# Optimization experiments

Measured on AMD Instinct MI355X. Metric: run time of the kernel, lower is better.

Reference implementation:

```python
import jax, jax.numpy as jnp
import numpy as np

N_EMB, D_LAT, D_HID, D_MID, D_IN = 1024, 64, 256, 128, 9
BETA = 0.25  # commitment_cost
N = 262144


def _kaiming(k, shape):
    # kaiming_normal_ with nonlinearity='relu': std = sqrt(2 / fan_in)
    fan_in = shape[1]
    return jax.random.normal(k, shape, jnp.float32) * jnp.sqrt(jnp.float32(2.0 / fan_in))


def setup_inputs() -> dict:
    key = jax.random.key(0)
    ks = jax.random.split(key, 8)
    return {
        "x": jax.random.normal(ks[0], (N, D_IN), jnp.float32),
        # Encoder: Linear(9->256) ReLU Linear(256->128) ReLU Linear(128->64)
        "enc_w1": _kaiming(ks[1], (D_HID, D_IN)),  "enc_b1": jnp.zeros((D_HID,), jnp.float32),
        "enc_w2": _kaiming(ks[2], (D_MID, D_HID)), "enc_b2": jnp.zeros((D_MID,), jnp.float32),
        "enc_w3": _kaiming(ks[3], (D_LAT, D_MID)), "enc_b3": jnp.zeros((D_LAT,), jnp.float32),
        # Decoder: Linear(64->128) ReLU Linear(128->256) ReLU Linear(256->9)
        "dec_w1": _kaiming(ks[4], (D_MID, D_LAT)), "dec_b1": jnp.zeros((D_MID,), jnp.float32),
        "dec_w2": _kaiming(ks[5], (D_HID, D_MID)), "dec_b2": jnp.zeros((D_HID,), jnp.float32),
        "dec_w3": _kaiming(ks[6], (D_IN, D_HID)),  "dec_b3": jnp.zeros((D_IN,), jnp.float32),
        # Codebook: Embedding(1024, 64), uniform(-1, 1)
        "codebook": jax.random.uniform(ks[7], (N_EMB, D_LAT), jnp.float32, -1.0, 1.0),
    }


def _mlp3(h, w1, b1, w2, b2, w3, b3):
    h = jax.nn.relu(h @ w1.T + b1)
    h = jax.nn.relu(h @ w2.T + b2)
    return h @ w3.T + b3


def reference(x, enc_w1, enc_b1, enc_w2, enc_b2, enc_w3, enc_b3,
              dec_w1, dec_b1, dec_w2, dec_b2, dec_w3, dec_b3, codebook):
    z_e = _mlp3(x, enc_w1, enc_b1, enc_w2, enc_b2, enc_w3, enc_b3)  # [N, 64]
    # squared euclidean distances to codebook: [N, N_EMB]
    d = (jnp.sum(z_e * z_e, axis=1, keepdims=True)
         - 2.0 * (z_e @ codebook.T)
         + jnp.sum(codebook * codebook, axis=1))
    idx = jnp.argmin(d, axis=1)                 # [N] int
    quantized = codebook[idx]                   # gather == onehot @ codebook
    e_latent = jnp.mean((jax.lax.stop_gradient(quantized) - z_e) ** 2)
    q_latent = jnp.mean((quantized - jax.lax.stop_gradient(z_e)) ** 2)
    vq_loss = q_latent + BETA * e_latent
    # straight-through estimator
    z_q = z_e + jax.lax.stop_gradient(quantized - z_e)
    # perplexity from codebook usage histogram (== mean of one-hot encodings)
    counts = jnp.zeros((N_EMB,), jnp.float32).at[idx].add(1.0)
    avg_probs = counts / jnp.float32(z_e.shape[0])
    perplexity = jnp.exp(-jnp.sum(avg_probs * jnp.log(avg_probs + 1e-10)))
    x_recon = _mlp3(z_q, dec_w1, dec_b1, dec_w2, dec_b2, dec_w3, dec_b3)
    return (x_recon, vq_loss, perplexity)
```

## Files before the change

kernel.cpp:

```cpp
#include <hip/hip_runtime.h>
#include <math.h>


namespace {

constexpr int kN = 262144;

typedef _Float16 half8 __attribute__((ext_vector_type(8)));
typedef float floatx4 __attribute__((ext_vector_type(4)));

#define MFMA16(a, b, c) __builtin_amdgcn_mfma_f32_16x16x32_f16((a), (b), (c), 0, 0, 0)
#define LDS_FENCE() asm volatile("s_waitcnt lgkmcnt(0)" ::: "memory")
#define VMCNT0() asm volatile("s_waitcnt vmcnt(0)" ::: "memory")
#define BARRIER()                                  \
  do {                                             \
    asm volatile("" ::: "memory");                 \
    __builtin_amdgcn_s_barrier();                  \
    asm volatile("" ::: "memory");                 \
  } while (0)

constexpr size_t W1M_O = 0;
constexpr size_t W1R_O = 16384;
constexpr size_t E2M_O = 32768;
constexpr size_t E2R_O = 98304;
constexpr size_t E3M_O = 163840;
constexpr size_t E3R_O = 180224;
constexpr size_t CBM_O = 196608;
constexpr size_t CBR_O = 327680;
constexpr size_t D1P_O = 458752;
constexpr size_t D2P_O = 475136;
constexpr size_t D3P_O = 540672;
constexpr size_t CN_O  = 548864;
constexpr size_t IDX_O = 589824;
constexpr size_t ESP_O = IDX_O + 1048576;
constexpr size_t HP_O  = ESP_O + 32768;

__device__ __forceinline__ void split2(float v, _Float16& hi, _Float16& lo) {
  hi = (_Float16)v;
  lo = (_Float16)(v - (float)hi);
}

__global__ void prep_kernel(
    const float* __restrict__ ew1, const float* __restrict__ ew2,
    const float* __restrict__ ew3, const float* __restrict__ cb,
    const float* __restrict__ dw1, const float* __restrict__ dw2,
    const float* __restrict__ dw3, char* __restrict__ wsb) {
  _Float16* w1m = (_Float16*)(wsb + W1M_O);
  _Float16* w1r = (_Float16*)(wsb + W1R_O);
  _Float16* e2m = (_Float16*)(wsb + E2M_O);
  _Float16* e2r = (_Float16*)(wsb + E2R_O);
  _Float16* e3m = (_Float16*)(wsb + E3M_O);
  _Float16* e3r = (_Float16*)(wsb + E3R_O);
  _Float16* cbm = (_Float16*)(wsb + CBM_O);
  _Float16* cbr = (_Float16*)(wsb + CBR_O);
  _Float16* d1p = (_Float16*)(wsb + D1P_O);
  _Float16* d2p = (_Float16*)(wsb + D2P_O);
  _Float16* d3p = (_Float16*)(wsb + D3P_O);
  float* cn = (float*)(wsb + CN_O);

  const int gid = blockIdx.x * 256 + threadIdx.x;
  const int stride = gridDim.x * 256;
  for (int e = gid; e < 256 * 32; e += stride) {
    int n = e >> 5, k = e & 31;
    float v = (k < 9) ? ew1[n * 9 + k] : 0.f;
    split2(v, w1m[e], w1r[e]);
  }
  for (int e = gid; e < 128 * 256; e += stride) split2(ew2[e], e2m[e], e2r[e]);
  for (int e = gid; e < 64 * 128; e += stride) split2(ew3[e], e3m[e], e3r[e]);
  for (int e = gid; e < 1024 * 64; e += stride) split2(cb[e], cbm[e], cbr[e]);
  for (int e = gid; e < 128 * 64; e += stride) d1p[e] = (_Float16)dw1[e];
  for (int e = gid; e < 256 * 128; e += stride) d2p[e] = (_Float16)dw2[e];
  for (int e = gid; e < 16 * 256; e += stride) {
    int n = e >> 8, k = e & 255;
    d3p[e] = (n < 9) ? (_Float16)dw3[n * 256 + k] : (_Float16)0.f;
  }
  for (int i = gid; i < 1024; i += stride) {
    float s = 0.f;
    const float* c = cb + (size_t)i * 64;
#pragma unroll 8
    for (int k = 0; k < 64; ++k) s = fmaf(c[k], c[k], s);
    cn[i] = s;
  }
}

__global__ __launch_bounds__(256, 3) void vqvae_mega(
    const float* __restrict__ x,
    const float* __restrict__ eb1, const float* __restrict__ eb2,
    const float* __restrict__ eb3, const float* __restrict__ db1,
    const float* __restrict__ db2, const float* __restrict__ db3,
    const float* __restrict__ cb, const char* __restrict__ wsb,
    float* __restrict__ out, int* __restrict__ idx_g, float* __restrict__ esp_g) {
  __shared__ _Float16 LP[20480];

  const int t = threadIdx.x;
  const int lane = t & 63;
  const int w = t >> 6;
  const int m = lane & 15;
  const int q = lane >> 4;
  const int R0 = blockIdx.x * 128;
  const int wr0 = 32 * w;
  _Float16* WPS = LP + 10240 + w * 2560;
  const float* cn_g = (const float*)(wsb + CN_O);

  half8 axm[2] = {{}, {}}, axr[2] = {{}, {}};
#pragma unroll
  for (int rt = 0; rt < 2; ++rt) {
    const int grow = R0 + wr0 + 16 * rt + m;
    if (q == 0) {
#pragma unroll
      for (int j = 0; j < 8; ++j) {
        const float v = x[(size_t)grow * 9 + j];
        const _Float16 hi = (_Float16)v;
        axm[rt][j] = hi;
        axr[rt][j] = (_Float16)(v - (float)hi);
      }
    } else if (q == 1) {
      const float v = x[(size_t)grow * 9 + 8];
      const _Float16 hi = (_Float16)v;
      axm[rt][0] = hi;
      axr[rt][0] = (_Float16)(v - (float)hi);
    }
  }

  floatx4 acc2[8][2];
#pragma unroll
  for (int nt = 0; nt < 8; ++nt)
#pragma unroll
    for (int rt = 0; rt < 2; ++rt) acc2[nt][rt] = (floatx4){0.f, 0.f, 0.f, 0.f};

  {
    const int pA = t >> 7, nA = t & 127;
    const char* srcA = wsb + (pA ? E2R_O : E2M_O) + (size_t)nA * 512;
    _Float16* dstA = LP + (pA ? 5120 : 0) + nA * 40;
    half8 stg[4];
#pragma unroll
    for (int j = 0; j < 4; ++j) stg[j] = *(const half8*)(srcA + j * 16);

    for (int kc = 0; kc < 8; ++kc) {
      VMCNT0();
#pragma unroll
      for (int j = 0; j < 4; ++j) *(half8*)(dstA + j * 8) = stg[j];
      LDS_FENCE();
      if (kc < 7) {
#pragma unroll
        for (int j = 0; j < 4; ++j)
          stg[j] = *(const half8*)(srcA + (size_t)(kc + 1) * 64 + j * 16);
      }
      BARRIER();

#pragma unroll
      for (int ntl = 0; ntl < 2; ++ntl) {
        const int f = kc * 32 + ntl * 16 + m;
        const half8 bm = *(const half8*)(wsb + W1M_O + (size_t)f * 64 + q * 16);
        const half8 br = *(const half8*)(wsb + W1R_O + (size_t)f * 64 + q * 16);
        const float bias = eb1[f];
#pragma unroll
        for (int rt = 0; rt < 2; ++rt) {
          floatx4 a = (floatx4){0.f, 0.f, 0.f, 0.f};
          a = MFMA16(axr[rt], bm, a);
          a = MFMA16(axm[rt], br, a);
          a = MFMA16(axm[rt], bm, a);
#pragma unroll
          for (int reg = 0; reg < 4; ++reg) {
            const float v = fmaxf(a[reg] + bias, 0.f);
            const int row = 16 * rt + 4 * q + reg;
            const _Float16 hi = (_Float16)v;
            WPS[row * 40 + ntl * 16 + m] = hi;
            WPS[1280 + row * 40 + ntl * 16 + m] = (_Float16)(v - (float)hi);
          }
        }
      }
      LDS_FENCE();
      half8 am[2], ar[2];
#pragma unroll
      for (int rt = 0; rt < 2; ++rt) {
        am[rt] = *(const half8*)(WPS + (16 * rt + m) * 40 + q * 8);
        ar[rt] = *(const half8*)(WPS + 1280 + (16 * rt + m) * 40 + q * 8);
      }
#pragma unroll
      for (int nt = 0; nt < 8; ++nt) {
        const half8 bm = *(const half8*)(LP + (nt * 16 + m) * 40 + q * 8);
        const half8 br = *(const half8*)(LP + 5120 + (nt * 16 + m) * 40 + q * 8);
#pragma unroll
        for (int rt = 0; rt < 2; ++rt) {
          acc2[nt][rt] = MFMA16(ar[rt], bm, acc2[nt][rt]);
          acc2[nt][rt] = MFMA16(am[rt], br, acc2[nt][rt]);
          acc2[nt][rt] = MFMA16(am[rt], bm, acc2[nt][rt]);
        }
      }
      BARRIER();
    }
  }

  floatx4 acc3[4][2];
#pragma unroll
  for (int nt = 0; nt < 4; ++nt)
#pragma unroll
    for (int rt = 0; rt < 2; ++rt) acc3[nt][rt] = (floatx4){0.f, 0.f, 0.f, 0.f};

  for (int ks = 0; ks < 4; ++ks) {
#pragma unroll
    for (int h = 0; h < 2; ++h) {
      const int nt = 2 * ks + h;
      const float bias = eb2[nt * 16 + m];
#pragma unroll
      for (int rt = 0; rt < 2; ++rt) {
#pragma unroll
        for (int reg = 0; reg < 4; ++reg) {
          const float v = fmaxf(acc2[nt][rt][reg] + bias, 0.f);
          const int row = 16 * rt + 4 * q + reg;
          const _Float16 hi = (_Float16)v;
          WPS[row * 40 + h * 16 + m] = hi;
          WPS[1280 + row * 40 + h * 16 + m] = (_Float16)(v - (float)hi);
        }
      }
    }
    LDS_FENCE();
    half8 am[2], ar[2];
#pragma unroll
    for (int rt = 0; rt < 2; ++rt) {
      am[rt] = *(const half8*)(WPS + (16 * rt + m) * 40 + q * 8);
      ar[rt] = *(const half8*)(WPS + 1280 + (16 * rt + m) * 40 + q * 8);
    }
#pragma unroll
    for (int nt = 0; nt < 4; ++nt) {
      const half8 bm = *(const half8*)(wsb + E3M_O + (size_t)(nt * 16 + m) * 256 + ks * 64 + q * 16);
      const half8 br = *(const half8*)(wsb + E3R_O + (size_t)(nt * 16 + m) * 256 + ks * 64 + q * 16);
#pragma unroll
      for (int rt = 0; rt < 2; ++rt) {
        acc3[nt][rt] = MFMA16(ar[rt], bm, acc3[nt][rt]);
        acc3[nt][rt] = MFMA16(am[rt], br, acc3[nt][rt]);
        acc3[nt][rt] = MFMA16(am[rt], bm, acc3[nt][rt]);
      }
    }
  }

  const int pC = t >> 7, eC = t & 127;
  const int nC = eC >> 1, hC = eC & 1;
  const char* srcC = wsb + (pC ? CBR_O : CBM_O) + (size_t)nC * 128 + hC * 64;
  _Float16* dstC = LP + (pC ? 4608 : 0) + nC * 72 + hC * 32;
  half8 stgC[4];
#pragma unroll
  for (int j = 0; j < 4; ++j) stgC[j] = *(const half8*)(srcC + j * 16);

  half8 zfm[2][2], zfr[2][2];
#pragma unroll
  for (int rt = 0; rt < 2; ++rt) {
#pragma unroll
    for (int nt = 0; nt < 4; ++nt) {
      const float bias = eb3[nt * 16 + m];
#pragma unroll
      for (int reg = 0; reg < 4; ++reg) {
        const float v = acc3[nt][rt][reg] + bias;
        const int row = 4 * q + reg;
        const _Float16 hi = (_Float16)v;
        WPS[row * 72 + nt * 16 + m] = hi;
        WPS[1152 + row * 72 + nt * 16 + m] = (_Float16)(v - (float)hi);
      }
    }
    LDS_FENCE();
#pragma unroll
    for (int ks2 = 0; ks2 < 2; ++ks2) {
      zfm[rt][ks2] = *(const half8*)(WPS + m * 72 + ks2 * 32 + q * 8);
      zfr[rt][ks2] = *(const half8*)(WPS + 1152 + m * 72 + ks2 * 32 + q * 8);
    }
  }

  float bestd[2][4];
  int besti[2][4];
#pragma unroll
  for (int rt = 0; rt < 2; ++rt)
#pragma unroll
    for (int reg = 0; reg < 4; ++reg) { bestd[rt][reg] = 3.4e38f; besti[rt][reg] = 0; }

  for (int cc = 0; cc < 16; ++cc) {
    VMCNT0();
#pragma unroll
    for (int j = 0; j < 4; ++j) *(half8*)(dstC + j * 8) = stgC[j];
    LDS_FENCE();
    if (cc < 15) {
#pragma unroll
      for (int j = 0; j < 4; ++j)
        stgC[j] = *(const half8*)(srcC + (size_t)(cc + 1) * 8192 + j * 16);
    }
    BARRIER();

    floatx4 accd[4][2];
#pragma unroll
    for (int nt = 0; nt < 4; ++nt)
#pragma unroll
      for (int rt = 0; rt < 2; ++rt) accd[nt][rt] = (floatx4){0.f, 0.f, 0.f, 0.f};
#pragma unroll
    for (int nt = 0; nt < 4; ++nt) {
#pragma unroll
      for (int ks2 = 0; ks2 < 2; ++ks2) {
        const half8 bm = *(const half8*)(LP + (nt * 16 + m) * 72 + ks2 * 32 + q * 8);
        const half8 br = *(const half8*)(LP + 4608 + (nt * 16 + m) * 72 + ks2 * 32 + q * 8);
#pragma unroll
        for (int rt = 0; rt < 2; ++rt) {
          accd[nt][rt] = MFMA16(zfr[rt][ks2], bm, accd[nt][rt]);
          accd[nt][rt] = MFMA16(zfm[rt][ks2], br, accd[nt][rt]);
          accd[nt][rt] = MFMA16(zfm[rt][ks2], bm, accd[nt][rt]);
        }
      }
    }
#pragma unroll
    for (int nt = 0; nt < 4; ++nt) {
      const int code = cc * 64 + nt * 16 + m;
      const float cnv = cn_g[code];
#pragma unroll
      for (int rt = 0; rt < 2; ++rt) {
#pragma unroll
        for (int reg = 0; reg < 4; ++reg) {
          const float d = cnv - 2.f * accd[nt][rt][reg];
          if (d < bestd[rt][reg]) { bestd[rt][reg] = d; besti[rt][reg] = code; }
        }
      }
    }
    BARRIER();
  }
#pragma unroll
  for (int rt = 0; rt < 2; ++rt) {
#pragma unroll
    for (int reg = 0; reg < 4; ++reg) {
#pragma unroll
      for (int off = 1; off < 16; off <<= 1) {
        const float od = __shfl_xor(bestd[rt][reg], off, 16);
        const int oi = __shfl_xor(besti[rt][reg], off, 16);
        if (od < bestd[rt][reg] || (od == bestd[rt][reg] && oi < besti[rt][reg])) {
          bestd[rt][reg] = od; besti[rt][reg] = oi;
        }
      }
    }
  }
  if (m == 0) {
#pragma unroll
    for (int rt = 0; rt < 2; ++rt)
#pragma unroll
      for (int reg = 0; reg < 4; ++reg) {
        const int row = wr0 + 16 * rt + 4 * q + reg;
        idx_g[R0 + row] = besti[rt][reg];
      }
  }

  const int sl = ((m >> 2) << 4) | m;
  half8 zq[2][2];
  float es = 0.f;
#pragma unroll
  for (int rt = 0; rt < 2; ++rt) {
    const int b0 = __shfl(besti[rt][0], sl);
    const int b1 = __shfl(besti[rt][1], sl);
    const int b2 = __shfl(besti[rt][2], sl);
    const int b3 = __shfl(besti[rt][3], sl);
    const int r2 = m & 3;
    const int bi = (r2 == 0) ? b0 : (r2 == 1) ? b1 : (r2 == 2) ? b2 : b3;
#pragma unroll
    for (int ks2 = 0; ks2 < 2; ++ks2) {
      const float* cp = cb + (size_t)bi * 64 + ks2 * 32 + q * 8;
      const float4 c0 = *(const float4*)cp;
      const float4 c1 = *(const float4*)(cp + 4);
      float cv[8] = {c0.x, c0.y, c0.z, c0.w, c1.x, c1.y, c1.z, c1.w};
#pragma unroll
      for (int j = 0; j < 8; ++j) {
        const float z = (float)zfm[rt][ks2][j] + (float)zfr[rt][ks2][j];
        const float d = cv[j] - z;
        es = fmaf(d, d, es);
        zq[rt][ks2][j] = (_Float16)(z + d);
      }
    }
  }
#pragma unroll
  for (int off = 1; off < 64; off <<= 1) es += __shfl_xor(es, off, 64);
  if (lane == 0) esp_g[blockIdx.x * 4 + w] = es;

  const int nE = t >> 2, jE = t & 3;
  const char* srcE = wsb + D2P_O + (size_t)nE * 256 + jE * 64;
  _Float16* dstE = LP + nE * 136 + jE * 32;
  half8 stgE[4];
#pragma unroll
  for (int j = 0; j < 4; ++j) stgE[j] = *(const half8*)(srcE + j * 16);

  floatx4 accH[8][2];
#pragma unroll
  for (int nt = 0; nt < 8; ++nt)
#pragma unroll
    for (int rt = 0; rt < 2; ++rt) accH[nt][rt] = (floatx4){0.f, 0.f, 0.f, 0.f};
#pragma unroll
  for (int nt = 0; nt < 8; ++nt) {
#pragma unroll
    for (int ks2 = 0; ks2 < 2; ++ks2) {
      const half8 b = *(const half8*)(wsb + D1P_O + (size_t)(nt * 16 + m) * 128 + ks2 * 64 + q * 16);
#pragma unroll
      for (int rt = 0; rt < 2; ++rt) accH[nt][rt] = MFMA16(zq[rt][ks2], b, accH[nt][rt]);
    }
  }
  half8 h3f[2][4];
  for (int ks = 0; ks < 4; ++ks) {
#pragma unroll
    for (int h = 0; h < 2; ++h) {
      const int nt = 2 * ks + h;
      const float bias = db1[nt * 16 + m];
#pragma unroll
      for (int rt = 0; rt < 2; ++rt)
#pragma unroll
        for (int reg = 0; reg < 4; ++reg) {
          const float v = fmaxf(accH[nt][rt][reg] + bias, 0.f);
          WPS[(16 * rt + 4 * q + reg) * 40 + h * 16 + m] = (_Float16)v;
        }
    }
    LDS_FENCE();
#pragma unroll
    for (int rt = 0; rt < 2; ++rt)
      h3f[rt][ks] = *(const half8*)(WPS + (16 * rt + m) * 40 + q * 8);
  }

  floatx4 accO[2] = {(floatx4){0.f, 0.f, 0.f, 0.f}, (floatx4){0.f, 0.f, 0.f, 0.f}};
  for (int jc = 0; jc < 4; ++jc) {
    VMCNT0();
#pragma unroll
    for (int j = 0; j < 4; ++j) *(half8*)(dstE + j * 8) = stgE[j];
    LDS_FENCE();
    if (jc < 3) {
#pragma unroll
      for (int j = 0; j < 4; ++j)
        stgE[j] = *(const half8*)(srcE + (size_t)(jc + 1) * 16384 + j * 16);
    }
    BARRIER();

    floatx4 accD2[4][2];
#pragma unroll
    for (int nt = 0; nt < 4; ++nt)
#pragma unroll
      for (int rt = 0; rt < 2; ++rt) accD2[nt][rt] = (floatx4){0.f, 0.f, 0.f, 0.f};
#pragma unroll
    for (int nt = 0; nt < 4; ++nt) {
#pragma unroll
      for (int ks = 0; ks < 4; ++ks) {
        const half8 b = *(const half8*)(LP + (nt * 16 + m) * 136 + ks * 32 + q * 8);
#pragma unroll
        for (int rt = 0; rt < 2; ++rt) accD2[nt][rt] = MFMA16(h3f[rt][ks], b, accD2[nt][rt]);
      }
    }
    half8 b3[2];
#pragma unroll
    for (int ks2 = 0; ks2 < 2; ++ks2)
      b3[ks2] = *(const half8*)(wsb + D3P_O + (size_t)m * 512 + jc * 128 + ks2 * 64 + q * 16);
#pragma unroll
    for (int rt = 0; rt < 2; ++rt) {
#pragma unroll
      for (int nt = 0; nt < 4; ++nt) {
        const float bias = db2[jc * 64 + nt * 16 + m];
#pragma unroll
        for (int reg = 0; reg < 4; ++reg) {
          const float v = fmaxf(accD2[nt][rt][reg] + bias, 0.f);
          WPS[(4 * q + reg) * 72 + nt * 16 + m] = (_Float16)v;
        }
      }
      LDS_FENCE();
#pragma unroll
      for (int ks2 = 0; ks2 < 2; ++ks2) {
        const half8 am = *(const half8*)(WPS + m * 72 + ks2 * 32 + q * 8);
        accO[rt] = MFMA16(am, b3[ks2], accO[rt]);
      }
    }
    BARRIER();
  }
  if (m < 9) {
    const float bias = db3[m];
#pragma unroll
    for (int rt = 0; rt < 2; ++rt)
#pragma unroll
      for (int reg = 0; reg < 4; ++reg) {
        const size_t r = (size_t)(R0 + wr0 + 16 * rt + 4 * q + reg);
        out[r * 9 + m] = accO[rt][reg] + bias;
      }
  }
}

__global__ __launch_bounds__(256) void hist_kernel(
    const int* __restrict__ idx_g, int* __restrict__ hp) {
  __shared__ int lh[1024];
  const int t = threadIdx.x;
#pragma unroll
  for (int i = 0; i < 4; ++i) lh[t * 4 + i] = 0;
  __syncthreads();
  for (int i = t; i < 4096; i += 256)
    atomicAdd(&lh[idx_g[blockIdx.x * 4096 + i]], 1);
  __syncthreads();
  int* part = hp + blockIdx.x * 1024;
#pragma unroll
  for (int i = 0; i < 4; ++i) part[t * 4 + i] = lh[t * 4 + i];
}

__global__ __launch_bounds__(1024) void finalize_kernel(
    const int* __restrict__ hp, const float* __restrict__ esp,
    float* __restrict__ out2) {
  __shared__ double red[1024];
  __shared__ float rede[1024];
  const int t = threadIdx.x;
  int h = 0;
#pragma unroll 8
  for (int p = 0; p < 64; ++p) h += hp[p * 1024 + t];
  const float pr = (float)h * (1.0f / (float)kN);
  red[t] = (double)(pr * logf(pr + 1e-10f));
  float es = 0.f;
#pragma unroll
  for (int i = 0; i < 8; ++i) es += esp[i * 1024 + t];
  rede[t] = es;
  __syncthreads();
  for (int s = 512; s > 0; s >>= 1) {
    if (t < s) { red[t] += red[t + s]; rede[t] += rede[t + s]; }
    __syncthreads();
  }
  if (t == 0) {
    out2[0] = 1.25f * (rede[0] * (1.0f / ((float)kN * 64.0f)));
    out2[1] = expf((float)(-red[0]));
  }
}

}

extern "C" void kernel_launch(void* const* d_in, const int* in_sizes, int n_in,
                              void* d_out, int out_size, void* d_ws, size_t ws_size,
                              hipStream_t stream) {
  const float* x   = (const float*)d_in[0];
  const float* ew1 = (const float*)d_in[1];
  const float* eb1 = (const float*)d_in[2];
  const float* ew2 = (const float*)d_in[3];
  const float* eb2 = (const float*)d_in[4];
  const float* ew3 = (const float*)d_in[5];
  const float* eb3 = (const float*)d_in[6];
  const float* dw1 = (const float*)d_in[7];
  const float* db1 = (const float*)d_in[8];
  const float* dw2 = (const float*)d_in[9];
  const float* db2 = (const float*)d_in[10];
  const float* dw3 = (const float*)d_in[11];
  const float* db3 = (const float*)d_in[12];
  const float* cb  = (const float*)d_in[13];
  float* out = (float*)d_out;
  char* wsb = (char*)d_ws;

  int* idx_g = (int*)(wsb + IDX_O);
  float* esp = (float*)(wsb + ESP_O);
  int* hp = (int*)(wsb + HP_O);

  prep_kernel<<<128, 256, 0, stream>>>(ew1, ew2, ew3, cb, dw1, dw2, dw3, wsb);
  vqvae_mega<<<kN / 128, 256, 0, stream>>>(x, eb1, eb2, eb3, db1, db2, db3, cb,
                                           wsb, out, idx_g, esp);
  hist_kernel<<<64, 256, 0, stream>>>(idx_g, hp);
  finalize_kernel<<<1, 1024, 0, stream>>>(hp, esp, out + (size_t)kN * 9);
}
```

Baseline: 322.0 us.

## Double-buffer codebook and decoder LDS tiles with XOR swizzle and MFMA priority

The codebook-distance loop and the decoder layer-2 loop now stage their tiles into two alternating LDS buffers, so the trailing barrier in each iteration can go. The padded row strides (72 and 136) are replaced with unpadded strides and an XOR swizzle on the column offset, which aims to avoid LDS bank conflicts without wasting space. The MFMA sections are wrapped in s_setprio raises so matrix work gets scheduling priority over other waves. Shared memory per block grows from about 40 KB to 52 KB. That could limit blocks per CU at the launch bound of 3, and it adds dependence on correct buffer-reuse ordering.

```diff
diff --git a/kernel.cpp b/kernel.cpp
--- a/kernel.cpp
+++ b/kernel.cpp
@@ -90,7 +90,7 @@
     const float* __restrict__ db2, const float* __restrict__ db3,
     const float* __restrict__ cb, const char* __restrict__ wsb,
     float* __restrict__ out, int* __restrict__ idx_g, float* __restrict__ esp_g) {
-  __shared__ _Float16 LP[20480];
+  __shared__ _Float16 LP[26624];
 
   const int t = threadIdx.x;
   const int lane = t & 63;
@@ -99,8 +99,9 @@
   const int q = lane >> 4;
   const int R0 = blockIdx.x * 128;
   const int wr0 = 32 * w;
-  _Float16* WPS = LP + 10240 + w * 2560;
+  _Float16* WPS = LP + 16384 + w * 2560;
   const float* cn_g = (const float*)(wsb + CN_O);
+  const int swq = (m & 7) << 3;
 
   half8 axm[2] = {{}, {}}, axr[2] = {{}, {}};
 #pragma unroll
@@ -177,6 +178,7 @@
         am[rt] = *(const half8*)(WPS + (16 * rt + m) * 40 + q * 8);
         ar[rt] = *(const half8*)(WPS + 1280 + (16 * rt + m) * 40 + q * 8);
       }
+      __builtin_amdgcn_s_setprio(1);
 #pragma unroll
       for (int nt = 0; nt < 8; ++nt) {
         const half8 bm = *(const half8*)(LP + (nt * 16 + m) * 40 + q * 8);
@@ -188,6 +190,7 @@
           acc2[nt][rt] = MFMA16(am[rt], bm, acc2[nt][rt]);
         }
       }
+      __builtin_amdgcn_s_setprio(0);
       BARRIER();
     }
   }
@@ -238,7 +241,8 @@
   const int pC = t >> 7, eC = t & 127;
   const int nC = eC >> 1, hC = eC & 1;
   const char* srcC = wsb + (pC ? CBR_O : CBM_O) + (size_t)nC * 128 + hC * 64;
-  _Float16* dstC = LP + (pC ? 4608 : 0) + nC * 72 + hC * 32;
+  const int dCbase = pC * 4096 + nC * 64;
+  const int swC = (nC & 7) << 3;
   half8 stgC[4];
 #pragma unroll
   for (int j = 0; j < 4; ++j) stgC[j] = *(const half8*)(srcC + j * 16);
@@ -274,9 +278,14 @@
     for (int reg = 0; reg < 4; ++reg) { bestd[rt][reg] = 3.4e38f; besti[rt][reg] = 0; }
 
   for (int cc = 0; cc < 16; ++cc) {
+    const int bb = (cc & 1) << 13;
     VMCNT0();
-#pragma unroll
-    for (int j = 0; j < 4; ++j) *(half8*)(dstC + j * 8) = stgC[j];
+    {
+      _Float16* d0 = LP + bb + dCbase;
+#pragma unroll
+      for (int j = 0; j < 4; ++j)
+        *(half8*)(d0 + ((hC * 32 + j * 8) ^ swC)) = stgC[j];
+    }
     LDS_FENCE();
     if (cc < 15) {
 #pragma unroll
@@ -290,12 +299,14 @@
     for (int nt = 0; nt < 4; ++nt)
 #pragma unroll
       for (int rt = 0; rt < 2; ++rt) accd[nt][rt] = (floatx4){0.f, 0.f, 0.f, 0.f};
+    __builtin_amdgcn_s_setprio(1);
 #pragma unroll
     for (int nt = 0; nt < 4; ++nt) {
 #pragma unroll
       for (int ks2 = 0; ks2 < 2; ++ks2) {
-        const half8 bm = *(const half8*)(LP + (nt * 16 + m) * 72 + ks2 * 32 + q * 8);
-        const half8 br = *(const half8*)(LP + 4608 + (nt * 16 + m) * 72 + ks2 * 32 + q * 8);
+        const int ko = (ks2 * 32 + q * 8) ^ swq;
+        const half8 bm = *(const half8*)(LP + bb + (nt * 16 + m) * 64 + ko);
+        const half8 br = *(const half8*)(LP + bb + 4096 + (nt * 16 + m) * 64 + ko);
 #pragma unroll
         for (int rt = 0; rt < 2; ++rt) {
           accd[nt][rt] = MFMA16(zfr[rt][ks2], bm, accd[nt][rt]);
@@ -304,6 +315,7 @@
         }
       }
     }
+    __builtin_amdgcn_s_setprio(0);
 #pragma unroll
     for (int nt = 0; nt < 4; ++nt) {
       const int code = cc * 64 + nt * 16 + m;
@@ -317,7 +329,6 @@
         }
       }
     }
-    BARRIER();
   }
 #pragma unroll
   for (int rt = 0; rt < 2; ++rt) {
@@ -375,7 +386,8 @@
 
   const int nE = t >> 2, jE = t & 3;
   const char* srcE = wsb + D2P_O + (size_t)nE * 256 + jE * 64;
-  _Float16* dstE = LP + nE * 136 + jE * 32;
+  const int dEbase = nE * 128;
+  const int swE = (nE & 7) << 3;
   half8 stgE[4];
 #pragma unroll
   for (int j = 0; j < 4; ++j) stgE[j] = *(const half8*)(srcE + j * 16);
@@ -385,6 +397,7 @@
   for (int nt = 0; nt < 8; ++nt)
 #pragma unroll
     for (int rt = 0; rt < 2; ++rt) accH[nt][rt] = (floatx4){0.f, 0.f, 0.f, 0.f};
+  __builtin_amdgcn_s_setprio(1);
 #pragma unroll
   for (int nt = 0; nt < 8; ++nt) {
 #pragma unroll
@@ -394,6 +407,7 @@
       for (int rt = 0; rt < 2; ++rt) accH[nt][rt] = MFMA16(zq[rt][ks2], b, accH[nt][rt]);
     }
   }
+  __builtin_amdgcn_s_setprio(0);
   half8 h3f[2][4];
   for (int ks = 0; ks < 4; ++ks) {
 #pragma unroll
@@ -416,9 +430,14 @@
 
   floatx4 accO[2] = {(floatx4){0.f, 0.f, 0.f, 0.f}, (floatx4){0.f, 0.f, 0.f, 0.f}};
   for (int jc = 0; jc < 4; ++jc) {
+    const int bb = (jc & 1) << 13;
     VMCNT0();
-#pragma unroll
-    for (int j = 0; j < 4; ++j) *(half8*)(dstE + j * 8) = stgE[j];
+    {
+      _Float16* d0 = LP + bb + dEbase;
+#pragma unroll
+      for (int j = 0; j < 4; ++j)
+        *(half8*)(d0 + ((jE * 32 + j * 8) ^ swE)) = stgE[j];
+    }
     LDS_FENCE();
     if (jc < 3) {
 #pragma unroll
@@ -432,15 +451,17 @@
     for (int nt = 0; nt < 4; ++nt)
 #pragma unroll
       for (int rt = 0; rt < 2; ++rt) accD2[nt][rt] = (floatx4){0.f, 0.f, 0.f, 0.f};
+    __builtin_amdgcn_s_setprio(1);
 #pragma unroll
     for (int nt = 0; nt < 4; ++nt) {
 #pragma unroll
       for (int ks = 0; ks < 4; ++ks) {
-        const half8 b = *(const half8*)(LP + (nt * 16 + m) * 136 + ks * 32 + q * 8);
+        const half8 b = *(const half8*)(LP + bb + (nt * 16 + m) * 128 + ((ks * 32 + q * 8) ^ swq));
 #pragma unroll
         for (int rt = 0; rt < 2; ++rt) accD2[nt][rt] = MFMA16(h3f[rt][ks], b, accD2[nt][rt]);
       }
     }
+    __builtin_amdgcn_s_setprio(0);
     half8 b3[2];
 #pragma unroll
     for (int ks2 = 0; ks2 < 2; ++ks2)
@@ -463,7 +484,6 @@
         accO[rt] = MFMA16(am, b3[ks2], accO[rt]);
       }
     }
-    BARRIER();
   }
   if (m < 9) {
     const float bias = db3[m];
```

After: 330.4 us. 1.03x slower.
